# Performance work log

Measured on AMD Instinct MI355X. Metric: run time of the kernel, lower is better.

## Reference

```python
import jax, jax.numpy as jnp
import numpy as np

K_GAUSS = 7      # gaussian_kernel_size
K_CONV = 5       # base-kernel conv size
SIGMA_MIN = 0.01
SIGMA_MAX = 1.0


def setup_inputs() -> dict:
    key = jax.random.key(0)
    k1, k2, k3 = jax.random.split(key, 3)
    input_data = jax.random.normal(k1, (8, 3, 224, 224), dtype=jnp.float32)
    foa_xy = jax.random.randint(k2, (8, 2), 0, 224)  # (x=row, y=col) fixation per sample
    weight = jax.random.normal(k3, (64, 3, K_CONV, K_CONV), dtype=jnp.float32) * 0.05
    return {"input_data": input_data, "foa_xy": foa_xy, "weight": weight}


def _extract_patches(x, k):
    # torch.nn.functional.unfold with stride=1, dilation=1, padding=k//2
    # x: (b,c,h,w) -> (b,c,k*k,h*w); patch flat index = ki*k + kj (row-major)
    b, c, h, w = x.shape
    p = k // 2
    xp = jnp.pad(x, ((0, 0), (0, 0), (p, p), (p, p)))
    shifts = [xp[:, :, i:i + h, j:j + w] for i in range(k) for j in range(k)]
    return jnp.stack(shifts, axis=2).reshape(b, c, k * k, h * w)


def _gaussian_modulate(x, foa_xy):
    # GaussianFOAConv2d: per-pixel normalized Gaussian kernel, sigma linear in distance from FOA
    b, c, h, w = x.shape
    hw = h * w
    ii, jj = jnp.meshgrid(jnp.arange(h, dtype=jnp.float32),
                          jnp.arange(w, dtype=jnp.float32), indexing='ij')
    xy = jnp.stack([ii, jj], axis=-1).reshape(hw, 2)           # (hw,2): (row, col)
    foa = foa_xy.astype(jnp.float32)                            # (b,2)
    dists = jnp.linalg.norm(xy[None, :, :] - foa[:, None, :], axis=-1)
    dists = dists / np.float32(np.sqrt(h ** 2 + w ** 2))        # (b,hw) in [0,1]
    sigmas = (1.0 - dists) * SIGMA_MIN + dists * SIGMA_MAX      # (b,hw)
    r = jnp.arange(-(K_GAUSS // 2), K_GAUSS // 2 + 1, dtype=jnp.float32)
    d2 = (r[:, None] ** 2 + r[None, :] ** 2).reshape(-1)        # (kk,) row-major, matches patch order
    kern = jnp.exp(-d2[None, :, None] / (2.0 * sigmas[:, None, :] ** 2))  # (b,kk,hw)
    kern = kern / jnp.sum(kern, axis=1, keepdims=True)
    patches = _extract_patches(x, K_GAUSS)                      # (b,c,kk,hw)
    out = jnp.einsum('bckp,bkp->bcp', patches, kern)            # spatial-only kernel -> sum over kk
    return out.reshape(b, c, h, w)


def reference(input_data, foa_xy, weight):
    # 1) Gaussian input modulation driven by FOA distance
    modulated = _gaussian_modulate(input_data, foa_xy)
    # 2) classic convolution with the learnable base kernel (stride 1, 'same' padding, no bias)
    p = K_CONV // 2
    return jax.lax.conv_general_dilated(
        modulated, weight, window_strides=(1, 1), padding=((p, p), (p, p)),
        dimension_numbers=('NCHW', 'OIHW', 'NCHW'))
```

## Files before the change

### kernel.cpp

```cpp
#include <hip/hip_runtime.h>

#define H 224
#define W 224
#define HW (224 * 224)
#define CIN 3
#define OCH 64
#define PW 228
#define PHW (PW * PW)
#define MTW 32
#define MTH 16

typedef __attribute__((ext_vector_type(8))) short short8;
typedef __attribute__((ext_vector_type(4))) float f32x4;

__device__ __forceinline__ unsigned f2bf_pk(float lo, float hi) {
    unsigned a = __float_as_uint(lo), b = __float_as_uint(hi);
    a = (a + 0x7FFFu + ((a >> 16) & 1u)) >> 16;
    b = (b + 0x7FFFu + ((b >> 16) & 1u)) & 0xFFFF0000u;
    return a | b;
}

__global__ void make_wA(const float* __restrict__ w, uint4* __restrict__ wA) {
    int t = threadIdx.x;
    if (t >= 768) return;
    int lane = t & 63;
    int fi = t >> 6;
    int mt = fi / 3, ks = fi - mt * 3;
    int q = lane >> 4;
    int oc = mt * 16 + (lane & 15);
    float v[8];
#pragma unroll
    for (int j = 0; j < 8; ++j) {
        int kk = q * 8 + j;
        v[j] = (kk < 25) ? w[oc * 75 + ks * 25 + kk] : 0.f;
    }
    uint4 r;
    r.x = f2bf_pk(v[0], v[1]);
    r.y = f2bf_pk(v[2], v[3]);
    r.z = f2bf_pk(v[4], v[5]);
    r.w = f2bf_pk(v[6], v[7]);
    wA[fi * 64 + lane] = r;
}

__global__ __launch_bounds__(256) void modulate(
    const float* __restrict__ in, const int* __restrict__ foa,
    float* __restrict__ Pm)
{
    __shared__ float s_raw[CIN][MTH + 6][40];

    int tx0 = blockIdx.x * MTW;
    int ty0 = blockIdx.y * MTH;
    int b = blockIdx.z;
    int tid = threadIdx.x;

    const float* src = in + (size_t)b * CIN * HW;
    for (int i = tid; i < CIN * 22 * 38; i += 256) {
        int ch = i / (22 * 38);
        int rem = i - ch * (22 * 38);
        int rr = rem / 38;
        int cc = rem - rr * 38;
        int gr = ty0 - 3 + rr, gc = tx0 - 3 + cc;
        float v = 0.f;
        if ((unsigned)gr < H && (unsigned)gc < W) v = src[ch * HW + gr * W + gc];
        s_raw[ch][rr][cc] = v;
    }
    __syncthreads();

    float fr = (float)foa[2 * b + 0], fc = (float)foa[2 * b + 1];
    for (int p = tid; p < MTH * MTW; p += 256) {
        int r = p >> 5, c = p & 31;
        int gr = ty0 + r, gc = tx0 + c;
        float dr = (float)gr - fr, dc = (float)gc - fc;
        float dist = sqrtf(dr * dr + dc * dc) * 3.1567268e-3f;
        float sigma = 0.01f + 0.99f * dist;
        float ae = -0.5f / (sigma * sigma);
        float e1 = __expf(ae);
        float e2 = e1 * e1, e4 = e2 * e2, e9 = e4 * e4 * e1;
        float pw[7] = {e9, e4, e1, 1.f, e1, e4, e9};
        float S = 1.f + 2.f * (e1 + e4 + e9);
        float inv = 1.f / (S * S);
#pragma unroll
        for (int ch = 0; ch < CIN; ++ch) {
            float a = 0.f;
#pragma unroll
            for (int ki = 0; ki < 7; ++ki) {
                const float* rp = &s_raw[ch][r + ki][c];
                float rs = 0.f;
#pragma unroll
                for (int kj = 0; kj < 7; ++kj) rs += pw[kj] * rp[kj];
                a += pw[ki] * rs;
            }
            Pm[(size_t)(b * CIN + ch) * PHW + (size_t)(gr + 2) * PW + (gc + 2)] = a * inv;
        }
    }
}

__global__ __launch_bounds__(256, 4) void gemm(
    const uint4* __restrict__ wA, const float* __restrict__ Pm,
    float* __restrict__ out)
{
    int tid = threadIdx.x;
    int lane = tid & 63;
    int wv = tid >> 6;
    int q = lane >> 4, li = lane & 15;

    int px0 = blockIdx.x * 16;
    int py = blockIdx.y * 4 + wv;
    int b = blockIdx.z;

    short8 aw[4][3];
#pragma unroll
    for (int mt = 0; mt < 4; ++mt)
#pragma unroll
        for (int ks = 0; ks < 3; ++ks) {
            union { uint4 u4; short8 s8; } cv;
            cv.u4 = wA[(mt * 3 + ks) * 64 + lane];
            aw[mt][ks] = cv.s8;
        }

    int ofs[8];
#pragma unroll
    for (int j = 0; j < 8; ++j) {
        int kk = q * 8 + j;
        int kkc = kk > 24 ? 24 : kk;
        int ky = (kkc * 13) >> 6;
        int kx = kkc - ky * 5;
        ofs[j] = ky * PW + kx;
    }

    short8 bf[3];
#pragma unroll
    for (int ks = 0; ks < 3; ++ks) {
        const float* p = Pm + (size_t)(b * CIN + ks) * PHW + (size_t)py * PW + px0 + li;
        float v[8];
#pragma unroll
        for (int j = 0; j < 8; ++j) v[j] = p[ofs[j]];
        union { unsigned u[4]; short8 s8; } cv;
        cv.u[0] = f2bf_pk(v[0], v[1]);
        cv.u[1] = f2bf_pk(v[2], v[3]);
        cv.u[2] = f2bf_pk(v[4], v[5]);
        cv.u[3] = f2bf_pk(v[6], v[7]);
        bf[ks] = cv.s8;
    }

    f32x4 acc[4];
#pragma unroll
    for (int mt = 0; mt < 4; ++mt) acc[mt] = (f32x4){0.f, 0.f, 0.f, 0.f};
#pragma unroll
    for (int ks = 0; ks < 3; ++ks)
#pragma unroll
        for (int mt = 0; mt < 4; ++mt)
            acc[mt] = __builtin_amdgcn_mfma_f32_16x16x32_bf16(
                aw[mt][ks], bf[ks], acc[mt], 0, 0, 0);

#pragma unroll
    for (int mt = 0; mt < 4; ++mt) {
#pragma unroll
        for (int r = 0; r < 4; ++r) {
            int oc = mt * 16 + q * 4 + r;
            out[(size_t)(b * OCH + oc) * HW + (size_t)py * W + px0 + li] = acc[mt][r];
        }
    }
}

extern "C" void kernel_launch(void* const* d_in, const int* in_sizes, int n_in,
                              void* d_out, int out_size, void* d_ws, size_t ws_size,
                              hipStream_t stream) {
    const float* input  = (const float*)d_in[0];
    const int*   foa    = (const int*)d_in[1];
    const float* weight = (const float*)d_in[2];
    float* outp = (float*)d_out;

    uint4* wA = (uint4*)d_ws;
    float* Pm = (float*)((char*)d_ws + 16384);

    hipMemsetAsync(Pm, 0, (size_t)8 * CIN * PHW * sizeof(float), stream);

    make_wA<<<1, 768, 0, stream>>>(weight, wA);

    dim3 gridM(W / MTW, H / MTH, 8);
    modulate<<<gridM, 256, 0, stream>>>(input, foa, Pm);

    dim3 gridG(14, 56, 8);
    gemm<<<gridG, 256, 0, stream>>>(wA, Pm, outp);
}
```

Measured before the change: 137.5 us.

## Fuse gaussian modulation into conv GEMM kernel via shared-memory halo tiles

Merges the modulate and gemm kernels into one fused kernel. Each block loads a raw input halo tile, computes the modulated tile (with a 2-pixel halo, recomputed redundantly) into shared memory, then runs the bf16 MFMA conv directly from shared memory. This removes the padded intermediate buffer, its memset, a kernel launch, and the global round trip. In exchange, modulation is recomputed on overlapping halos and only 216 of 256 threads do the modulate phase.

Result: slower. 149.4 us (+8.6%).

```diff
diff --git a/kernel.cpp b/kernel.cpp
--- a/kernel.cpp
+++ b/kernel.cpp
@@ -5,10 +5,15 @@
 #define HW (224 * 224)
 #define CIN 3
 #define OCH 64
-#define PW 228
-#define PHW (PW * PW)
-#define MTW 32
-#define MTH 16
+
+#define BPX 32
+#define BPY 4
+#define RRW 14
+#define RCW 42
+#define RST 44
+#define MRW 8
+#define MCW 36
+#define MST 40
 
 typedef __attribute__((ext_vector_type(8))) short short8;
 typedef __attribute__((ext_vector_type(4))) float f32x4;
@@ -42,24 +47,25 @@
     wA[fi * 64 + lane] = r;
 }
 
-__global__ __launch_bounds__(256) void modulate(
-    const float* __restrict__ in, const int* __restrict__ foa,
-    float* __restrict__ Pm)
+__global__ __launch_bounds__(256, 4) void fused(
+    const uint4* __restrict__ wA, const float* __restrict__ in,
+    const int* __restrict__ foa, float* __restrict__ out)
 {
-    __shared__ float s_raw[CIN][MTH + 6][40];
-
-    int tx0 = blockIdx.x * MTW;
-    int ty0 = blockIdx.y * MTH;
+    __shared__ float s_raw[CIN][RRW][RST];
+    __shared__ float s_mod[CIN][MRW][MST];
+
+    int tid = threadIdx.x;
+    int px0 = blockIdx.x * BPX;
+    int py0 = blockIdx.y * BPY;
     int b = blockIdx.z;
-    int tid = threadIdx.x;
 
     const float* src = in + (size_t)b * CIN * HW;
-    for (int i = tid; i < CIN * 22 * 38; i += 256) {
-        int ch = i / (22 * 38);
-        int rem = i - ch * (22 * 38);
-        int rr = rem / 38;
-        int cc = rem - rr * 38;
-        int gr = ty0 - 3 + rr, gc = tx0 - 3 + cc;
+    for (int i = tid; i < CIN * RRW * RCW; i += 256) {
+        int ch = i / (RRW * RCW);
+        int rem = i - ch * (RRW * RCW);
+        int rr = rem / RCW;
+        int cc = rem - rr * RCW;
+        int gr = py0 - 5 + rr, gc = px0 - 5 + cc;
         float v = 0.f;
         if ((unsigned)gr < H && (unsigned)gc < W) v = src[ch * HW + gr * W + gc];
         s_raw[ch][rr][cc] = v;
@@ -67,46 +73,59 @@
     __syncthreads();
 
     float fr = (float)foa[2 * b + 0], fc = (float)foa[2 * b + 1];
-    for (int p = tid; p < MTH * MTW; p += 256) {
-        int r = p >> 5, c = p & 31;
-        int gr = ty0 + r, gc = tx0 + c;
-        float dr = (float)gr - fr, dc = (float)gc - fc;
-        float dist = sqrtf(dr * dr + dc * dc) * 3.1567268e-3f;
-        float sigma = 0.01f + 0.99f * dist;
-        float ae = -0.5f / (sigma * sigma);
-        float e1 = __expf(ae);
-        float e2 = e1 * e1, e4 = e2 * e2, e9 = e4 * e4 * e1;
-        float pw[7] = {e9, e4, e1, 1.f, e1, e4, e9};
-        float S = 1.f + 2.f * (e1 + e4 + e9);
-        float inv = 1.f / (S * S);
-#pragma unroll
-        for (int ch = 0; ch < CIN; ++ch) {
-            float a = 0.f;
-#pragma unroll
-            for (int ki = 0; ki < 7; ++ki) {
-                const float* rp = &s_raw[ch][r + ki][c];
+    if (tid < 216) {
+        int ch = tid / 72;
+        int rem = tid - ch * 72;
+        int r = rem / 9;
+        int qc = rem - r * 9;
+        int c0 = qc * 4;
+        int gm_r = py0 - 2 + r;
+
+        float pw[4][7], inv[4], acc[4] = {0.f, 0.f, 0.f, 0.f};
+#pragma unroll
+        for (int o = 0; o < 4; ++o) {
+            int gm_c = px0 - 2 + c0 + o;
+            float dr = (float)gm_r - fr, dc = (float)gm_c - fc;
+            float dist = sqrtf(dr * dr + dc * dc) * 3.1567268e-3f;
+            float sigma = 0.01f + 0.99f * dist;
+            float ae = -0.5f / (sigma * sigma);
+            float e1 = __expf(ae);
+            float e2 = e1 * e1, e4 = e2 * e2, e9 = e4 * e4 * e1;
+            pw[o][0] = e9; pw[o][1] = e4; pw[o][2] = e1; pw[o][3] = 1.f;
+            pw[o][4] = e1; pw[o][5] = e4; pw[o][6] = e9;
+            float S = 1.f + 2.f * (e1 + e4 + e9);
+            inv[o] = 1.f / (S * S);
+        }
+#pragma unroll
+        for (int ki = 0; ki < 7; ++ki) {
+            const float* rp = &s_raw[ch][r + ki][c0];
+            float rv[10];
+            *(f32x4*)&rv[0] = *(const f32x4*)&rp[0];
+            *(f32x4*)&rv[4] = *(const f32x4*)&rp[4];
+            rv[8] = rp[8]; rv[9] = rp[9];
+#pragma unroll
+            for (int o = 0; o < 4; ++o) {
                 float rs = 0.f;
 #pragma unroll
-                for (int kj = 0; kj < 7; ++kj) rs += pw[kj] * rp[kj];
-                a += pw[ki] * rs;
+                for (int kj = 0; kj < 7; ++kj) rs += pw[o][kj] * rv[o + kj];
+                acc[o] += pw[o][ki] * rs;
             }
-            Pm[(size_t)(b * CIN + ch) * PHW + (size_t)(gr + 2) * PW + (gc + 2)] = a * inv;
-        }
-    }
-}
-
-__global__ __launch_bounds__(256, 4) void gemm(
-    const uint4* __restrict__ wA, const float* __restrict__ Pm,
-    float* __restrict__ out)
-{
-    int tid = threadIdx.x;
+        }
+        float res[4];
+#pragma unroll
+        for (int o = 0; o < 4; ++o) {
+            int gm_c = px0 - 2 + c0 + o;
+            bool ok = ((unsigned)gm_r < H) && ((unsigned)gm_c < W);
+            res[o] = ok ? acc[o] * inv[o] : 0.f;
+        }
+        *(f32x4*)&s_mod[ch][r][c0] = *(const f32x4*)res;
+    }
+    __syncthreads();
+
     int lane = tid & 63;
     int wv = tid >> 6;
     int q = lane >> 4, li = lane & 15;
-
-    int px0 = blockIdx.x * 16;
-    int py = blockIdx.y * 4 + wv;
-    int b = blockIdx.z;
+    int py = py0 + wv;
 
     short8 aw[4][3];
 #pragma unroll
@@ -118,47 +137,51 @@
             aw[mt][ks] = cv.s8;
         }
 
-    int ofs[8];
+    int moff[8];
 #pragma unroll
     for (int j = 0; j < 8; ++j) {
         int kk = q * 8 + j;
         int kkc = kk > 24 ? 24 : kk;
         int ky = (kkc * 13) >> 6;
         int kx = kkc - ky * 5;
-        ofs[j] = ky * PW + kx;
-    }
-
-    short8 bf[3];
-#pragma unroll
-    for (int ks = 0; ks < 3; ++ks) {
-        const float* p = Pm + (size_t)(b * CIN + ks) * PHW + (size_t)py * PW + px0 + li;
-        float v[8];
-#pragma unroll
-        for (int j = 0; j < 8; ++j) v[j] = p[ofs[j]];
-        union { unsigned u[4]; short8 s8; } cv;
-        cv.u[0] = f2bf_pk(v[0], v[1]);
-        cv.u[1] = f2bf_pk(v[2], v[3]);
-        cv.u[2] = f2bf_pk(v[4], v[5]);
-        cv.u[3] = f2bf_pk(v[6], v[7]);
-        bf[ks] = cv.s8;
-    }
-
-    f32x4 acc[4];
-#pragma unroll
-    for (int mt = 0; mt < 4; ++mt) acc[mt] = (f32x4){0.f, 0.f, 0.f, 0.f};
-#pragma unroll
-    for (int ks = 0; ks < 3; ++ks)
-#pragma unroll
-        for (int mt = 0; mt < 4; ++mt)
-            acc[mt] = __builtin_amdgcn_mfma_f32_16x16x32_bf16(
-                aw[mt][ks], bf[ks], acc[mt], 0, 0, 0);
-
-#pragma unroll
-    for (int mt = 0; mt < 4; ++mt) {
-#pragma unroll
-        for (int r = 0; r < 4; ++r) {
-            int oc = mt * 16 + q * 4 + r;
-            out[(size_t)(b * OCH + oc) * HW + (size_t)py * W + px0 + li] = acc[mt][r];
+        moff[j] = (wv + ky) * MST + kx;
+    }
+
+#pragma unroll
+    for (int s = 0; s < 2; ++s) {
+        int sc = s * 16;
+        short8 bf[CIN];
+#pragma unroll
+        for (int ch = 0; ch < CIN; ++ch) {
+            const float* mp = &s_mod[ch][0][sc + li];
+            float v[8];
+#pragma unroll
+            for (int j = 0; j < 8; ++j) v[j] = mp[moff[j]];
+            union { unsigned u[4]; short8 s8; } cv;
+            cv.u[0] = f2bf_pk(v[0], v[1]);
+            cv.u[1] = f2bf_pk(v[2], v[3]);
+            cv.u[2] = f2bf_pk(v[4], v[5]);
+            cv.u[3] = f2bf_pk(v[6], v[7]);
+            bf[ch] = cv.s8;
+        }
+
+        f32x4 acc[4];
+#pragma unroll
+        for (int mt = 0; mt < 4; ++mt) acc[mt] = (f32x4){0.f, 0.f, 0.f, 0.f};
+#pragma unroll
+        for (int ch = 0; ch < CIN; ++ch)
+#pragma unroll
+            for (int mt = 0; mt < 4; ++mt)
+                acc[mt] = __builtin_amdgcn_mfma_f32_16x16x32_bf16(
+                    aw[mt][ch], bf[ch], acc[mt], 0, 0, 0);
+
+#pragma unroll
+        for (int mt = 0; mt < 4; ++mt) {
+#pragma unroll
+            for (int r = 0; r < 4; ++r) {
+                int oc = mt * 16 + q * 4 + r;
+                out[(size_t)(b * OCH + oc) * HW + (size_t)py * W + px0 + sc + li] = acc[mt][r];
+            }
         }
     }
 }
@@ -172,15 +195,9 @@
     float* outp = (float*)d_out;
 
     uint4* wA = (uint4*)d_ws;
-    float* Pm = (float*)((char*)d_ws + 16384);
-
-    hipMemsetAsync(Pm, 0, (size_t)8 * CIN * PHW * sizeof(float), stream);
 
     make_wA<<<1, 768, 0, stream>>>(weight, wA);
 
-    dim3 gridM(W / MTW, H / MTH, 8);
-    modulate<<<gridM, 256, 0, stream>>>(input, foa, Pm);
-
-    dim3 gridG(14, 56, 8);
-    gemm<<<gridG, 256, 0, stream>>>(wA, Pm, outp);
-}
+    dim3 grid(W / BPX, H / BPY, 8);
+    fused<<<grid, 256, 0, stream>>>(wA, input, foa, outp);
+}
```

## Fuse weight prep and border zeroing into modulate, store bf16 intermediate

Applied to the files above, without the earlier changes.

Weight packing moves into the first modulate block, and the memset is replaced by in-kernel zeroing of the padded borders, which removes two launches. The modulated image is stored as bf16 instead of fp32, halving intermediate traffic and removing the conversion in the GEMM. Modulate now uses 32x32 tiles with four pixels per thread and vectorized shared-memory row loads. The GEMM handles two 16-pixel subtiles per block, which reuses the weight registers. The workspace offset is shifted so the 8-byte bf16 stores stay aligned, and the intermediate loses some precision.

Result: faster. 130.3 us (-5.3%).

```diff
diff --git a/kernel.cpp b/kernel.cpp
--- a/kernel.cpp
+++ b/kernel.cpp
@@ -6,9 +6,11 @@
 #define CIN 3
 #define OCH 64
 #define PW 228
-#define PHW (PW * PW)
-#define MTW 32
-#define MTH 16
+#define PHW (228 * 228)
+
+#define MT 32
+#define RAWN 38
+#define RST 40
 
 typedef __attribute__((ext_vector_type(8))) short short8;
 typedef __attribute__((ext_vector_type(4))) float f32x4;
@@ -20,45 +22,45 @@
     return a | b;
 }
 
-__global__ void make_wA(const float* __restrict__ w, uint4* __restrict__ wA) {
-    int t = threadIdx.x;
-    if (t >= 768) return;
-    int lane = t & 63;
-    int fi = t >> 6;
-    int mt = fi / 3, ks = fi - mt * 3;
-    int q = lane >> 4;
-    int oc = mt * 16 + (lane & 15);
-    float v[8];
-#pragma unroll
-    for (int j = 0; j < 8; ++j) {
-        int kk = q * 8 + j;
-        v[j] = (kk < 25) ? w[oc * 75 + ks * 25 + kk] : 0.f;
-    }
-    uint4 r;
-    r.x = f2bf_pk(v[0], v[1]);
-    r.y = f2bf_pk(v[2], v[3]);
-    r.z = f2bf_pk(v[4], v[5]);
-    r.w = f2bf_pk(v[6], v[7]);
-    wA[fi * 64 + lane] = r;
-}
-
 __global__ __launch_bounds__(256) void modulate(
     const float* __restrict__ in, const int* __restrict__ foa,
-    float* __restrict__ Pm)
+    const float* __restrict__ w, ushort* __restrict__ Pm,
+    uint4* __restrict__ wA)
 {
-    __shared__ float s_raw[CIN][MTH + 6][40];
-
-    int tx0 = blockIdx.x * MTW;
-    int ty0 = blockIdx.y * MTH;
-    int b = blockIdx.z;
+    __shared__ float s_raw[CIN][RAWN][RST];
+
     int tid = threadIdx.x;
+    int bx = blockIdx.x, by = blockIdx.y, b = blockIdx.z;
+    int tx0 = bx * MT, ty0 = by * MT;
+
+    if ((bx | by | b) == 0) {
+        for (int t = tid; t < 768; t += 256) {
+            int lane = t & 63;
+            int fi = t >> 6;
+            int mt = fi / 3, ks = fi - mt * 3;
+            int q = lane >> 4;
+            int oc = mt * 16 + (lane & 15);
+            float v[8];
+#pragma unroll
+            for (int j = 0; j < 8; ++j) {
+                int kk = q * 8 + j;
+                v[j] = (kk < 25) ? w[oc * 75 + ks * 25 + kk] : 0.f;
+            }
+            uint4 r;
+            r.x = f2bf_pk(v[0], v[1]);
+            r.y = f2bf_pk(v[2], v[3]);
+            r.z = f2bf_pk(v[4], v[5]);
+            r.w = f2bf_pk(v[6], v[7]);
+            wA[fi * 64 + lane] = r;
+        }
+    }
 
     const float* src = in + (size_t)b * CIN * HW;
-    for (int i = tid; i < CIN * 22 * 38; i += 256) {
-        int ch = i / (22 * 38);
-        int rem = i - ch * (22 * 38);
-        int rr = rem / 38;
-        int cc = rem - rr * 38;
+    for (int i = tid; i < CIN * RAWN * RAWN; i += 256) {
+        int ch = i / (RAWN * RAWN);
+        int rem = i - ch * (RAWN * RAWN);
+        int rr = rem / RAWN;
+        int cc = rem - rr * RAWN;
         int gr = ty0 - 3 + rr, gc = tx0 - 3 + cc;
         float v = 0.f;
         if ((unsigned)gr < H && (unsigned)gc < W) v = src[ch * HW + gr * W + gc];
@@ -66,37 +68,81 @@
     }
     __syncthreads();
 
+    int r = tid >> 3, c0 = (tid & 7) << 2;
+    int gr = ty0 + r;
     float fr = (float)foa[2 * b + 0], fc = (float)foa[2 * b + 1];
-    for (int p = tid; p < MTH * MTW; p += 256) {
-        int r = p >> 5, c = p & 31;
-        int gr = ty0 + r, gc = tx0 + c;
+
+    float pw[4][7], inv[4];
+#pragma unroll
+    for (int o = 0; o < 4; ++o) {
+        int gc = tx0 + c0 + o;
         float dr = (float)gr - fr, dc = (float)gc - fc;
         float dist = sqrtf(dr * dr + dc * dc) * 3.1567268e-3f;
         float sigma = 0.01f + 0.99f * dist;
         float ae = -0.5f / (sigma * sigma);
         float e1 = __expf(ae);
         float e2 = e1 * e1, e4 = e2 * e2, e9 = e4 * e4 * e1;
-        float pw[7] = {e9, e4, e1, 1.f, e1, e4, e9};
+        pw[o][0] = e9; pw[o][1] = e4; pw[o][2] = e1; pw[o][3] = 1.f;
+        pw[o][4] = e1; pw[o][5] = e4; pw[o][6] = e9;
         float S = 1.f + 2.f * (e1 + e4 + e9);
-        float inv = 1.f / (S * S);
-#pragma unroll
-        for (int ch = 0; ch < CIN; ++ch) {
-            float a = 0.f;
-#pragma unroll
-            for (int ki = 0; ki < 7; ++ki) {
-                const float* rp = &s_raw[ch][r + ki][c];
+        inv[o] = 1.f / (S * S);
+    }
+
+    ushort* plane = Pm + (size_t)b * CIN * PHW;
+#pragma unroll
+    for (int ch = 0; ch < CIN; ++ch) {
+        float acc[4] = {0.f, 0.f, 0.f, 0.f};
+#pragma unroll
+        for (int ki = 0; ki < 7; ++ki) {
+            const float* rp = &s_raw[ch][r + ki][c0];
+            float rv[10];
+            *(float4*)&rv[0] = *(const float4*)rp;
+            *(float4*)&rv[4] = *(const float4*)(rp + 4);
+            *(float2*)&rv[8] = *(const float2*)(rp + 8);
+#pragma unroll
+            for (int o = 0; o < 4; ++o) {
                 float rs = 0.f;
 #pragma unroll
-                for (int kj = 0; kj < 7; ++kj) rs += pw[kj] * rp[kj];
-                a += pw[ki] * rs;
+                for (int kj = 0; kj < 7; ++kj) rs += pw[o][kj] * rv[o + kj];
+                acc[o] += pw[o][ki] * rs;
             }
-            Pm[(size_t)(b * CIN + ch) * PHW + (size_t)(gr + 2) * PW + (gc + 2)] = a * inv;
+        }
+        uint2 st;
+        st.x = f2bf_pk(acc[0] * inv[0], acc[1] * inv[1]);
+        st.y = f2bf_pk(acc[2] * inv[2], acc[3] * inv[3]);
+        *(uint2*)&plane[(size_t)ch * PHW + (size_t)(gr + 2) * PW + (tx0 + c0) + 2] = st;
+    }
+
+    if (by == 0 || by == 6) {
+        int pr0 = (by == 0) ? 0 : 226;
+        int cA = (bx == 0) ? -2 : tx0;
+        int cB = (bx == 6) ? 226 : tx0 + MT;
+        int n = cB - cA;
+        for (int i = tid; i < 2 * CIN * n; i += 256) {
+            int ch = i / (2 * n);
+            int rem = i - ch * 2 * n;
+            int rr = rem / n;
+            int c = cA + (rem - rr * n);
+            plane[(size_t)ch * PHW + (size_t)(pr0 + rr) * PW + c + 2] = 0;
+        }
+    }
+    if (bx == 0 || bx == 6) {
+        int cb = (bx == 0) ? -2 : 224;
+        int rA = (by == 0) ? 2 : ty0 + 2;
+        int rB = (by == 6) ? 226 : ty0 + 2 + MT;
+        int n = rB - rA;
+        for (int i = tid; i < 2 * CIN * n; i += 256) {
+            int ch = i / (2 * n);
+            int rem = i - ch * 2 * n;
+            int cc = rem / n;
+            int pr = rA + (rem - cc * n);
+            plane[(size_t)ch * PHW + (size_t)pr * PW + (cb + cc) + 2] = 0;
         }
     }
 }
 
 __global__ __launch_bounds__(256, 4) void gemm(
-    const uint4* __restrict__ wA, const float* __restrict__ Pm,
+    const uint4* __restrict__ wA, const ushort* __restrict__ Pm,
     float* __restrict__ out)
 {
     int tid = threadIdx.x;
@@ -104,7 +150,7 @@
     int wv = tid >> 6;
     int q = lane >> 4, li = lane & 15;
 
-    int px0 = blockIdx.x * 16;
+    int px0 = blockIdx.x * 32;
     int py = blockIdx.y * 4 + wv;
     int b = blockIdx.z;
 
@@ -128,37 +174,41 @@
         ofs[j] = ky * PW + kx;
     }
 
-    short8 bf[3];
-#pragma unroll
-    for (int ks = 0; ks < 3; ++ks) {
-        const float* p = Pm + (size_t)(b * CIN + ks) * PHW + (size_t)py * PW + px0 + li;
-        float v[8];
-#pragma unroll
-        for (int j = 0; j < 8; ++j) v[j] = p[ofs[j]];
-        union { unsigned u[4]; short8 s8; } cv;
-        cv.u[0] = f2bf_pk(v[0], v[1]);
-        cv.u[1] = f2bf_pk(v[2], v[3]);
-        cv.u[2] = f2bf_pk(v[4], v[5]);
-        cv.u[3] = f2bf_pk(v[6], v[7]);
-        bf[ks] = cv.s8;
-    }
-
-    f32x4 acc[4];
-#pragma unroll
-    for (int mt = 0; mt < 4; ++mt) acc[mt] = (f32x4){0.f, 0.f, 0.f, 0.f};
-#pragma unroll
-    for (int ks = 0; ks < 3; ++ks)
-#pragma unroll
-        for (int mt = 0; mt < 4; ++mt)
-            acc[mt] = __builtin_amdgcn_mfma_f32_16x16x32_bf16(
-                aw[mt][ks], bf[ks], acc[mt], 0, 0, 0);
-
-#pragma unroll
-    for (int mt = 0; mt < 4; ++mt) {
-#pragma unroll
-        for (int r = 0; r < 4; ++r) {
-            int oc = mt * 16 + q * 4 + r;
-            out[(size_t)(b * OCH + oc) * HW + (size_t)py * W + px0 + li] = acc[mt][r];
+#pragma unroll
+    for (int s = 0; s < 2; ++s) {
+        int px = px0 + s * 16 + li;
+        short8 bf[CIN];
+#pragma unroll
+        for (int ch = 0; ch < CIN; ++ch) {
+            const ushort* p = Pm + (size_t)(b * CIN + ch) * PHW + (size_t)py * PW + px;
+            unsigned v[8];
+#pragma unroll
+            for (int j = 0; j < 8; ++j) v[j] = p[ofs[j]];
+            union { unsigned u[4]; short8 s8; } cv;
+            cv.u[0] = v[0] | (v[1] << 16);
+            cv.u[1] = v[2] | (v[3] << 16);
+            cv.u[2] = v[4] | (v[5] << 16);
+            cv.u[3] = v[6] | (v[7] << 16);
+            bf[ch] = cv.s8;
+        }
+
+        f32x4 acc[4];
+#pragma unroll
+        for (int mt = 0; mt < 4; ++mt) acc[mt] = (f32x4){0.f, 0.f, 0.f, 0.f};
+#pragma unroll
+        for (int ch = 0; ch < CIN; ++ch)
+#pragma unroll
+            for (int mt = 0; mt < 4; ++mt)
+                acc[mt] = __builtin_amdgcn_mfma_f32_16x16x32_bf16(
+                    aw[mt][ch], bf[ch], acc[mt], 0, 0, 0);
+
+#pragma unroll
+        for (int mt = 0; mt < 4; ++mt) {
+#pragma unroll
+            for (int r = 0; r < 4; ++r) {
+                int oc = mt * 16 + q * 4 + r;
+                out[(size_t)(b * OCH + oc) * HW + (size_t)py * W + px] = acc[mt][r];
+            }
         }
     }
 }
@@ -171,16 +221,12 @@
     const float* weight = (const float*)d_in[2];
     float* outp = (float*)d_out;
 
-    uint4* wA = (uint4*)d_ws;
-    float* Pm = (float*)((char*)d_ws + 16384);
-
-    hipMemsetAsync(Pm, 0, (size_t)8 * CIN * PHW * sizeof(float), stream);
-
-    make_wA<<<1, 768, 0, stream>>>(weight, wA);
-
-    dim3 gridM(W / MTW, H / MTH, 8);
-    modulate<<<gridM, 256, 0, stream>>>(input, foa, Pm);
-
-    dim3 gridG(14, 56, 8);
+    uint4*  wA = (uint4*)d_ws;
+    ushort* Pm = (ushort*)((char*)d_ws + 16380);
+
+    dim3 gridM(W / MT, H / MT, 8);
+    modulate<<<gridM, 256, 0, stream>>>(input, foa, weight, Pm, wA);
+
+    dim3 gridG(7, 56, 8);
     gemm<<<gridG, 256, 0, stream>>>(wA, Pm, outp);
 }
```
